# Optimization experiments

Hardware: AMD Instinct MI355X
Metric: run time of the kernel (lower is better)

The kernel has to match this reference:

```python
import jax, jax.numpy as jnp
import numpy as np

VOCAB, EMBED, HIDDEN = 32000, 512, 1024
B, T = 8, 256

def setup_inputs() -> dict:
    key = jax.random.key(0)
    ks = jax.random.split(key, 5)
    x = jax.random.randint(ks[0], (B, T), 0, VOCAB)
    embedding = jax.random.normal(ks[1], (VOCAB, EMBED), dtype=jnp.float32)
    W_xh = jax.random.normal(ks[2], (EMBED, HIDDEN), dtype=jnp.float32) * 0.01
    W_hh = jax.random.normal(ks[3], (HIDDEN, HIDDEN), dtype=jnp.float32) * 0.01
    b_h = jnp.zeros((HIDDEN,), dtype=jnp.float32)
    W_hy = jax.random.normal(ks[4], (HIDDEN, VOCAB), dtype=jnp.float32) * 0.01
    b_y = jnp.zeros((VOCAB,), dtype=jnp.float32)
    return {"x": x, "embedding": embedding, "W_xh": W_xh, "W_hh": W_hh,
            "b_h": b_h, "W_hy": W_hy, "b_y": b_y}

def reference(x, embedding, W_xh, W_hh, b_h, W_hy, b_y):
    # x: [B,T] int ids
    emb = embedding[x]                      # [B,T,E]
    # Precompute input contribution for all steps: [B,T,H]
    xh = jnp.einsum('bte,eh->bth', emb, W_xh) + b_h
    h0 = jnp.zeros((x.shape[0], W_hh.shape[0]), dtype=emb.dtype)

    def step(h, xh_t):
        h = jnp.tanh(xh_t + h @ W_hh)       # [B,H]
        return h, h

    _, hs = jax.lax.scan(step, h0, jnp.swapaxes(xh, 0, 1))  # hs: [T,B,H]
    hs = jnp.swapaxes(hs, 0, 1)             # [B,T,H]
    # Output projection batched over all timesteps (same math as per-step)
    y = jnp.einsum('bth,hv->btv', hs, W_hy) + b_y  # [B,T,V]
    return y
```

## Files before the change

kernel.cpp:

```cpp
#include <hip/hip_runtime.h>
#include <hip/hip_bf16.h>

#define VOCAB 32000
#define EMBED 512
#define HIDDEN 1024
#define NB 8
#define NT 256
#define XH_ROWS 16

#define NCH 8
#define NMEM 32
#define RCOLS 32

typedef __attribute__((ext_vector_type(8))) short bf16x8;
typedef __attribute__((ext_vector_type(4))) float f32x4;

__device__ __forceinline__ unsigned short bf16_bits(float f) {
    __hip_bfloat16 b = __float2bfloat16(f);
    unsigned short s;
    __builtin_memcpy(&s, &b, 2);
    return s;
}

__global__ __launch_bounds__(256) void k_transpose(const float* __restrict__ W,
                                                   __hip_bfloat16* __restrict__ Wt) {
    __shared__ float tile[32][33];
    const int n0 = blockIdx.x * 32;
    const int k0 = blockIdx.y * 32;
    const int c = threadIdx.x & 31;
    const int r0 = threadIdx.x >> 5;
#pragma unroll
    for (int rr = 0; rr < 4; ++rr) {
        const int r = r0 + rr * 8;
        tile[c][r] = W[(size_t)(k0 + r) * VOCAB + n0 + c];
    }
    __syncthreads();
#pragma unroll
    for (int rr = 0; rr < 4; ++rr) {
        const int n = r0 + rr * 8;
        Wt[(size_t)(n0 + n) * HIDDEN + k0 + c] = __float2bfloat16(tile[n][c]);
    }
}

__global__ __launch_bounds__(256) void k_xh(const int* __restrict__ ids,
                                            const float* __restrict__ emb,
                                            const float* __restrict__ Wxh,
                                            const float* __restrict__ bh,
                                            float* __restrict__ xh) {
    __shared__ alignas(16) float embS[XH_ROWS][EMBED];
    __shared__ int idsS[XH_ROWS];
    const int tid = threadIdx.x;
    const int blk = blockIdx.x;
    if (tid < XH_ROWS) idsS[tid] = ids[blk * XH_ROWS + tid];
    __syncthreads();
    const float4* emb4 = (const float4*)emb;
#pragma unroll
    for (int rep = 0; rep < (XH_ROWS * EMBED / 4) / 256; ++rep) {
        const int lin = rep * 256 + tid;
        const int r = lin >> 7;
        const int e4 = lin & 127;
        *(float4*)&embS[r][e4 * 4] = emb4[(size_t)idsS[r] * (EMBED / 4) + e4];
    }
    __syncthreads();
    float4 acc[XH_ROWS] = {};
    const float4* W4 = (const float4*)Wxh;
    for (int e = 0; e < EMBED; ++e) {
        const float4 w = W4[(size_t)e * (HIDDEN / 4) + tid];
#pragma unroll
        for (int r = 0; r < XH_ROWS; ++r) {
            const float ev = embS[r][e];
            acc[r].x += ev * w.x; acc[r].y += ev * w.y;
            acc[r].z += ev * w.z; acc[r].w += ev * w.w;
        }
    }
    const float4 bv = ((const float4*)bh)[tid];
#pragma unroll
    for (int r = 0; r < XH_ROWS; ++r) {
        float4 o;
        o.x = acc[r].x + bv.x; o.y = acc[r].y + bv.y;
        o.z = acc[r].z + bv.z; o.w = acc[r].w + bv.w;
        ((float4*)xh)[(size_t)(blk * XH_ROWS + r) * (HIDDEN / 4) + tid] = o;
    }
}

__global__ __launch_bounds__(256, 1) void k_rec(const float* __restrict__ Whh,
                                                const float* __restrict__ xh,
                                                unsigned long long* __restrict__ hx,
                                                __hip_bfloat16* __restrict__ hs) {
    __shared__ unsigned WstU[16 * 1032];
    __shared__ float xhS[NT * RCOLS];
    __shared__ float hS[16 * 68];
    __shared__ float red[16 * 33];
    const int tid = threadIdx.x;
    const int bid = blockIdx.x;
    const int c = bid & (NCH - 1);
    const int m = bid >> 3;
    const int j0 = m * RCOLS;
    unsigned long long* hxc = hx + (size_t)c * 1024;

    if (tid < 16)
        __hip_atomic_store(&hxc[512 + m * 16 + tid], 0ull, __ATOMIC_RELAXED,
                           __HIP_MEMORY_SCOPE_AGENT);

    for (int lin = tid; lin < 16 * 64 * 16; lin += 256) {
        const int part = lin >> 10;
        const int rem = lin & 1023;
        const int ii = rem >> 4;
        const int col2 = rem & 15;
        const int i = part * 64 + ii;
        const float2 w = *(const float2*)&Whh[(size_t)i * HIDDEN + j0 + 2 * col2];
        WstU[part * 1032 + ii * 16 + col2] =
            (unsigned)bf16_bits(w.x) | ((unsigned)bf16_bits(w.y) << 16);
    }
    for (int idx = tid; idx < NT * RCOLS; idx += 256) {
        const int t = idx >> 5;
        const int col = idx & 31;
        xhS[idx] = xh[(size_t)(c * NT + t) * HIDDEN + j0 + col];
    }
    __syncthreads();

    const int col2 = tid & 15;
    const int part = tid >> 4;
    const unsigned* Wp = &WstU[part * 1032 + col2];
    const float* hp = &hS[part * 68];
    const int w0 = tid;
    const int w1 = tid + 256;
    const int pe0 = 2 * tid + 4 * (tid >> 5);

    for (int t = 0; t < NT; ++t) {
        unsigned long long* rbuf = hxc + ((t + 1) & 1) * 512;
        unsigned long long* wbuf = hxc + (t & 1) * 512;
        const unsigned long long tok = (unsigned long long)(unsigned)t;
        unsigned long long a = __hip_atomic_load(&rbuf[w0], __ATOMIC_RELAXED, __HIP_MEMORY_SCOPE_AGENT);
        unsigned long long b = __hip_atomic_load(&rbuf[w1], __ATOMIC_RELAXED, __HIP_MEMORY_SCOPE_AGENT);
        while (((a & 0xffffull) != tok) | ((b & 0xffffull) != tok)) {
            __builtin_amdgcn_s_sleep(1);
            if ((a & 0xffffull) != tok)
                a = __hip_atomic_load(&rbuf[w0], __ATOMIC_RELAXED, __HIP_MEMORY_SCOPE_AGENT);
            if ((b & 0xffffull) != tok)
                b = __hip_atomic_load(&rbuf[w1], __ATOMIC_RELAXED, __HIP_MEMORY_SCOPE_AGENT);
        }
        *(float2*)&hS[pe0] = make_float2(__uint_as_float(((unsigned)(a >> 16) & 0xffffu) << 16),
                                         __uint_as_float(((unsigned)(a >> 32) & 0xffffu) << 16));
        *(float2*)&hS[pe0 + 544] = make_float2(__uint_as_float(((unsigned)(b >> 16) & 0xffffu) << 16),
                                               __uint_as_float(((unsigned)(b >> 32) & 0xffffu) << 16));
        __syncthreads();
        float a0 = 0.f, a1 = 0.f;
#pragma unroll 8
        for (int ii = 0; ii < 64; ++ii) {
            const unsigned u = Wp[ii * 16];
            const float hv = hp[ii];
            a0 = fmaf(__uint_as_float(u << 16), hv, a0);
            a1 = fmaf(__uint_as_float(u & 0xffff0000u), hv, a1);
        }
        red[part * 33 + 2 * col2]     = a0;
        red[part * 33 + 2 * col2 + 1] = a1;
        __syncthreads();
        if (tid < RCOLS) {
            float s = 0.f;
#pragma unroll
            for (int p = 0; p < 16; ++p) s += red[p * 33 + tid];
            const float v = tanhf(xhS[t * RCOLS + tid] + s);
            const unsigned hb = (unsigned)bf16_bits(v);
            ((unsigned short*)hs)[(size_t)(c * NT + t) * HIDDEN + j0 + tid] = (unsigned short)hb;
            const unsigned pb = (unsigned)__shfl_xor((int)hb, 1, 64);
            if ((tid & 1) == 0) {
                const unsigned long long wv = (unsigned long long)(unsigned)(t + 1)
                                            | ((unsigned long long)hb << 16)
                                            | ((unsigned long long)pb << 32);
                __hip_atomic_store(&wbuf[m * 16 + (tid >> 1)], wv, __ATOMIC_RELAXED,
                                   __HIP_MEMORY_SCOPE_AGENT);
            }
        }
    }
}

__global__ __launch_bounds__(256) void k_proj(const __hip_bfloat16* __restrict__ A,
                                              const __hip_bfloat16* __restrict__ Bt,
                                              const float* __restrict__ by,
                                              float* __restrict__ C) {
    __shared__ __hip_bfloat16 At[128 * 32];
    __shared__ __hip_bfloat16 Bts[128 * 32];
    const int tid = threadIdx.x;
    const int lin = blockIdx.x;
    const int swz = (lin & 7) * 500 + (lin >> 3);
    const int m0 = (swz & 15) * 128;
    const int n0 = (swz >> 4) * 128;
    const int lane = tid & 63;
    const int w = tid >> 6;
    const int wr = w >> 1, wc = w & 1;
    const int fr = lane & 15, fq = lane >> 4;
    f32x4 acc[4][4] = {};
    for (int k0 = 0; k0 < HIDDEN; k0 += 32) {
#pragma unroll
        for (int i = 0; i < 2; ++i) {
            const int ch = i * 256 + tid;
            const int row = ch >> 2, kq = (ch & 3) * 8;
            const __hip_bfloat16* ga = A  + (size_t)(m0 + row) * HIDDEN + k0 + kq;
            const __hip_bfloat16* gb = Bt + (size_t)(n0 + row) * HIDDEN + k0 + kq;
            __hip_bfloat16* la = At  + (size_t)((i * 256 + w * 64) * 8);
            __hip_bfloat16* lb = Bts + (size_t)((i * 256 + w * 64) * 8);
            __builtin_amdgcn_global_load_lds((const __attribute__((address_space(1))) unsigned*)ga,
                                             (__attribute__((address_space(3))) unsigned*)la, 16, 0, 0);
            __builtin_amdgcn_global_load_lds((const __attribute__((address_space(1))) unsigned*)gb,
                                             (__attribute__((address_space(3))) unsigned*)lb, 16, 0, 0);
        }
        __syncthreads();
        bf16x8 af[4], bfr[4];
#pragma unroll
        for (int mm = 0; mm < 4; ++mm)
            af[mm] = *(const bf16x8*)&At[(wr * 64 + mm * 16 + fr) * 32 + fq * 8];
#pragma unroll
        for (int nn = 0; nn < 4; ++nn)
            bfr[nn] = *(const bf16x8*)&Bts[(wc * 64 + nn * 16 + fr) * 32 + fq * 8];
#pragma unroll
        for (int mm = 0; mm < 4; ++mm)
#pragma unroll
            for (int nn = 0; nn < 4; ++nn)
                acc[mm][nn] = __builtin_amdgcn_mfma_f32_16x16x32_bf16(af[mm], bfr[nn], acc[mm][nn], 0, 0, 0);
        __syncthreads();
    }
#pragma unroll
    for (int nn = 0; nn < 4; ++nn) {
        const int col = n0 + wc * 64 + nn * 16 + fr;
        const float bias = by[col];
#pragma unroll
        for (int mm = 0; mm < 4; ++mm) {
            const int row = m0 + wr * 64 + mm * 16 + fq * 4;
            float* cp = C + (size_t)row * VOCAB + col;
            cp[0]                 = acc[mm][nn][0] + bias;
            cp[(size_t)VOCAB]     = acc[mm][nn][1] + bias;
            cp[(size_t)2 * VOCAB] = acc[mm][nn][2] + bias;
            cp[(size_t)3 * VOCAB] = acc[mm][nn][3] + bias;
        }
    }
}

extern "C" void kernel_launch(void* const* d_in, const int* in_sizes, int n_in,
                              void* d_out, int out_size, void* d_ws, size_t ws_size,
                              hipStream_t stream) {
    const int*   x   = (const int*)d_in[0];
    const float* emb = (const float*)d_in[1];
    const float* Wxh = (const float*)d_in[2];
    const float* Whh = (const float*)d_in[3];
    const float* bh  = (const float*)d_in[4];
    const float* Why = (const float*)d_in[5];
    const float* by  = (const float*)d_in[6];
    float* y = (float*)d_out;

    char* ws = (char*)d_ws;
    const size_t off_xh = 0;
    const size_t off_hx = off_xh + (size_t)NB * NT * HIDDEN * 4;
    const size_t off_hs = off_hx + (size_t)NCH * 2 * 512 * 8;
    const size_t off_wt = off_hs + (size_t)NB * NT * HIDDEN * 2;
    const size_t need   = off_wt + (size_t)VOCAB * HIDDEN * 2;
    if (ws_size < need) return;

    float* xh = (float*)(ws + off_xh);
    unsigned long long* hx = (unsigned long long*)(ws + off_hx);
    __hip_bfloat16* hs = (__hip_bfloat16*)(ws + off_hs);
    __hip_bfloat16* Wt = (__hip_bfloat16*)(ws + off_wt);

    k_xh<<<dim3((NB * NT) / XH_ROWS), 256, 0, stream>>>(x, emb, Wxh, bh, xh);
    k_transpose<<<dim3(VOCAB / 32, HIDDEN / 32), 256, 0, stream>>>(Why, Wt);
    k_rec<<<dim3(NCH * NMEM), 256, 0, stream>>>(Whh, xh, hx, hs);
    k_proj<<<dim3((NB * NT / 128) * (VOCAB / 128)), 256, 0, stream>>>(hs, Wt, by, y);
}
```

Measured before the change: 982.0 us.

## Add fast-path mirrored exchange buffer with inline-asm polling for recurrent sync

The recurrent kernel's cross-block hidden-state exchange now writes every packet to two buffers: the original agent-scope one and a mirror written with workgroup-scope stores. Readers poll the mirror first using inline global_load_dwordx4 with sc0 and no sleep, and fall back to agent-scope loads with sleep after three misses. Only the upper 128 threads poll, each loading 16-byte vectors, which cuts per-thread load count and the latency of each step's spin-wait. It relies on hardware cache coherence behaviour that scope semantics do not guarantee. It also adds a second store per packet and a shared-memory padding change.

```diff
diff --git a/kernel.cpp b/kernel.cpp
--- a/kernel.cpp
+++ b/kernel.cpp
@@ -14,12 +14,34 @@
 
 typedef __attribute__((ext_vector_type(8))) short bf16x8;
 typedef __attribute__((ext_vector_type(4))) float f32x4;
+typedef __attribute__((ext_vector_type(4))) unsigned u32x4;
 
 __device__ __forceinline__ unsigned short bf16_bits(float f) {
     __hip_bfloat16 b = __float2bfloat16(f);
     unsigned short s;
     __builtin_memcpy(&s, &b, 2);
     return s;
+}
+
+__device__ __forceinline__ void fast_load2(u32x4& q0, u32x4& q1,
+                                           const unsigned long long* p0,
+                                           const unsigned long long* p1) {
+    asm volatile("global_load_dwordx4 %0, %2, off sc0\n\t"
+                 "global_load_dwordx4 %1, %3, off sc0\n\t"
+                 "s_waitcnt vmcnt(0)"
+                 : "=&v"(q0), "=&v"(q1)
+                 : "v"(p0), "v"(p1)
+                 : "memory");
+}
+__device__ __forceinline__ void fast_load1(u32x4& q, const unsigned long long* p) {
+    asm volatile("global_load_dwordx4 %0, %1, off sc0\n\ts_waitcnt vmcnt(0)"
+                 : "=&v"(q) : "v"(p) : "memory");
+}
+__device__ __forceinline__ void agent_load(u32x4& q, const unsigned long long* p) {
+    const unsigned long long a0 = __hip_atomic_load(p,     __ATOMIC_RELAXED, __HIP_MEMORY_SCOPE_AGENT);
+    const unsigned long long a1 = __hip_atomic_load(p + 1, __ATOMIC_RELAXED, __HIP_MEMORY_SCOPE_AGENT);
+    q.x = (unsigned)a0; q.y = (unsigned)(a0 >> 32);
+    q.z = (unsigned)a1; q.w = (unsigned)(a1 >> 32);
 }
 
 __global__ __launch_bounds__(256) void k_transpose(const float* __restrict__ W,
@@ -85,9 +107,10 @@
 
 __global__ __launch_bounds__(256, 1) void k_rec(const float* __restrict__ Whh,
                                                 const float* __restrict__ xh,
-                                                unsigned long long* __restrict__ hx,
+                                                unsigned long long* __restrict__ hxA,
+                                                unsigned long long* __restrict__ hxF,
                                                 __hip_bfloat16* __restrict__ hs) {
-    __shared__ unsigned WstU[16 * 1032];
+    __shared__ unsigned WstU[16 * 1040];
     __shared__ float xhS[NT * RCOLS];
     __shared__ float hS[16 * 68];
     __shared__ float red[16 * 33];
@@ -96,11 +119,15 @@
     const int c = bid & (NCH - 1);
     const int m = bid >> 3;
     const int j0 = m * RCOLS;
-    unsigned long long* hxc = hx + (size_t)c * 1024;
-
-    if (tid < 16)
-        __hip_atomic_store(&hxc[512 + m * 16 + tid], 0ull, __ATOMIC_RELAXED,
+    unsigned long long* hxcA = hxA + (size_t)c * 1024;
+    unsigned long long* hxcF = hxF + (size_t)c * 1024;
+
+    if (tid < 16) {
+        __hip_atomic_store(&hxcA[512 + m * 16 + tid], 0ull, __ATOMIC_RELAXED,
                            __HIP_MEMORY_SCOPE_AGENT);
+        __hip_atomic_store(&hxcF[512 + m * 16 + tid], 0ull, __ATOMIC_RELAXED,
+                           __HIP_MEMORY_SCOPE_WORKGROUP);
+    }
 
     for (int lin = tid; lin < 16 * 64 * 16; lin += 256) {
         const int part = lin >> 10;
@@ -109,7 +136,7 @@
         const int col2 = rem & 15;
         const int i = part * 64 + ii;
         const float2 w = *(const float2*)&Whh[(size_t)i * HIDDEN + j0 + 2 * col2];
-        WstU[part * 1032 + ii * 16 + col2] =
+        WstU[part * 1040 + ii * 16 + col2] =
             (unsigned)bf16_bits(w.x) | ((unsigned)bf16_bits(w.y) << 16);
     }
     for (int idx = tid; idx < NT * RCOLS; idx += 256) {
@@ -121,37 +148,55 @@
 
     const int col2 = tid & 15;
     const int part = tid >> 4;
-    const unsigned* Wp = &WstU[part * 1032 + col2];
+    const unsigned* Wp = &WstU[part * 1040 + col2];
     const float* hp = &hS[part * 68];
-    const int w0 = tid;
-    const int w1 = tid + 256;
-    const int pe0 = 2 * tid + 4 * (tid >> 5);
+    const int u = tid - 128;
 
     for (int t = 0; t < NT; ++t) {
-        unsigned long long* rbuf = hxc + ((t + 1) & 1) * 512;
-        unsigned long long* wbuf = hxc + (t & 1) * 512;
-        const unsigned long long tok = (unsigned long long)(unsigned)t;
-        unsigned long long a = __hip_atomic_load(&rbuf[w0], __ATOMIC_RELAXED, __HIP_MEMORY_SCOPE_AGENT);
-        unsigned long long b = __hip_atomic_load(&rbuf[w1], __ATOMIC_RELAXED, __HIP_MEMORY_SCOPE_AGENT);
-        while (((a & 0xffffull) != tok) | ((b & 0xffffull) != tok)) {
-            __builtin_amdgcn_s_sleep(1);
-            if ((a & 0xffffull) != tok)
-                a = __hip_atomic_load(&rbuf[w0], __ATOMIC_RELAXED, __HIP_MEMORY_SCOPE_AGENT);
-            if ((b & 0xffffull) != tok)
-                b = __hip_atomic_load(&rbuf[w1], __ATOMIC_RELAXED, __HIP_MEMORY_SCOPE_AGENT);
-        }
-        *(float2*)&hS[pe0] = make_float2(__uint_as_float(((unsigned)(a >> 16) & 0xffffu) << 16),
-                                         __uint_as_float(((unsigned)(a >> 32) & 0xffffu) << 16));
-        *(float2*)&hS[pe0 + 544] = make_float2(__uint_as_float(((unsigned)(b >> 16) & 0xffffu) << 16),
-                                               __uint_as_float(((unsigned)(b >> 32) & 0xffffu) << 16));
+        const int roff = ((t + 1) & 1) * 512;
+        const int woff = (t & 1) * 512;
+        const unsigned tk = (unsigned)t;
+        if (tid >= 128) {
+            const unsigned long long* pF = hxcF + roff + 4 * u;
+            const unsigned long long* pA = hxcA + roff + 4 * u;
+            u32x4 q0, q1;
+            fast_load2(q0, q1, pF, pF + 2);
+            int tries = 0;
+            while (true) {
+                const bool miss0 = ((q0.x & 0xffffu) != tk) | ((q0.z & 0xffffu) != tk);
+                const bool miss1 = ((q1.x & 0xffffu) != tk) | ((q1.z & 0xffffu) != tk);
+                if (!(miss0 | miss1)) break;
+                ++tries;
+                if (tries <= 3) {
+                    if (miss0) fast_load1(q0, pF);
+                    if (miss1) fast_load1(q1, pF + 2);
+                } else {
+                    __builtin_amdgcn_s_sleep(1);
+                    if (miss0) agent_load(q0, pA);
+                    if (miss1) agent_load(q1, pA + 2);
+                }
+            }
+            const int base = 8 * u + 4 * (u >> 3);
+            float4 f0, f1;
+            f0.x = __uint_as_float(q0.x & 0xffff0000u);
+            f0.y = __uint_as_float(q0.y << 16);
+            f0.z = __uint_as_float(q0.z & 0xffff0000u);
+            f0.w = __uint_as_float(q0.w << 16);
+            f1.x = __uint_as_float(q1.x & 0xffff0000u);
+            f1.y = __uint_as_float(q1.y << 16);
+            f1.z = __uint_as_float(q1.z & 0xffff0000u);
+            f1.w = __uint_as_float(q1.w << 16);
+            *(float4*)&hS[base] = f0;
+            *(float4*)&hS[base + 4] = f1;
+        }
         __syncthreads();
         float a0 = 0.f, a1 = 0.f;
 #pragma unroll 8
         for (int ii = 0; ii < 64; ++ii) {
-            const unsigned u = Wp[ii * 16];
+            const unsigned w = Wp[ii * 16];
             const float hv = hp[ii];
-            a0 = fmaf(__uint_as_float(u << 16), hv, a0);
-            a1 = fmaf(__uint_as_float(u & 0xffff0000u), hv, a1);
+            a0 = fmaf(__uint_as_float(w << 16), hv, a0);
+            a1 = fmaf(__uint_as_float(w & 0xffff0000u), hv, a1);
         }
         red[part * 33 + 2 * col2]     = a0;
         red[part * 33 + 2 * col2 + 1] = a1;
@@ -168,8 +213,10 @@
                 const unsigned long long wv = (unsigned long long)(unsigned)(t + 1)
                                             | ((unsigned long long)hb << 16)
                                             | ((unsigned long long)pb << 32);
-                __hip_atomic_store(&wbuf[m * 16 + (tid >> 1)], wv, __ATOMIC_RELAXED,
+                __hip_atomic_store(&hxcA[woff + m * 16 + (tid >> 1)], wv, __ATOMIC_RELAXED,
                                    __HIP_MEMORY_SCOPE_AGENT);
+                __hip_atomic_store(&hxcF[woff + m * 16 + (tid >> 1)], wv, __ATOMIC_RELAXED,
+                                   __HIP_MEMORY_SCOPE_WORKGROUP);
             }
         }
     }
@@ -249,20 +296,22 @@
     float* y = (float*)d_out;
 
     char* ws = (char*)d_ws;
-    const size_t off_xh = 0;
-    const size_t off_hx = off_xh + (size_t)NB * NT * HIDDEN * 4;
-    const size_t off_hs = off_hx + (size_t)NCH * 2 * 512 * 8;
-    const size_t off_wt = off_hs + (size_t)NB * NT * HIDDEN * 2;
-    const size_t need   = off_wt + (size_t)VOCAB * HIDDEN * 2;
+    const size_t off_xh  = 0;
+    const size_t off_hxa = off_xh + (size_t)NB * NT * HIDDEN * 4;
+    const size_t off_hxf = off_hxa + (size_t)NCH * 2 * 512 * 8;
+    const size_t off_hs  = off_hxf + (size_t)NCH * 2 * 512 * 8;
+    const size_t off_wt  = off_hs + (size_t)NB * NT * HIDDEN * 2;
+    const size_t need    = off_wt + (size_t)VOCAB * HIDDEN * 2;
     if (ws_size < need) return;
 
     float* xh = (float*)(ws + off_xh);
-    unsigned long long* hx = (unsigned long long*)(ws + off_hx);
+    unsigned long long* hxA = (unsigned long long*)(ws + off_hxa);
+    unsigned long long* hxF = (unsigned long long*)(ws + off_hxf);
     __hip_bfloat16* hs = (__hip_bfloat16*)(ws + off_hs);
     __hip_bfloat16* Wt = (__hip_bfloat16*)(ws + off_wt);
 
     k_xh<<<dim3((NB * NT) / XH_ROWS), 256, 0, stream>>>(x, emb, Wxh, bh, xh);
     k_transpose<<<dim3(VOCAB / 32, HIDDEN / 32), 256, 0, stream>>>(Why, Wt);
-    k_rec<<<dim3(NCH * NMEM), 256, 0, stream>>>(Whh, xh, hx, hs);
+    k_rec<<<dim3(NCH * NMEM), 256, 0, stream>>>(Whh, xh, hxA, hxF, hs);
     k_proj<<<dim3((NB * NT / 128) * (VOCAB / 128)), 256, 0, stream>>>(hs, Wt, by, y);
 }
```

Result: slower. 1.043 ms (+6.2%).
